# Kernel tuning notes

Hardware: AMD Instinct MI355X
Metric: run time of the kernel (lower is better)

The kernel has to match this reference:

```python
import jax, jax.numpy as jnp
import numpy as np

N = 131072        # total nodes in batched graph
E = 2097152       # total edges (avg degree 16)
F_IN = 256        # input feature dim
DIMS = [64, 32, 16]
G = 128           # number of graphs in batch


def setup_inputs() -> dict:
    key = jax.random.key(0)
    ks = jax.random.split(key, 16)
    inp = {
        "features": jax.random.normal(ks[0], (N, F_IN), jnp.float32),
        "src": jax.random.randint(ks[1], (E,), 0, N),
        "dst": jax.random.randint(ks[2], (E,), 0, N),
        "graph_ids": jnp.sort(jax.random.randint(ks[3], (N,), 0, G)),
    }
    d = F_IN
    for i, out in enumerate(DIMS):
        inp[f"W{i}"] = jax.random.normal(ks[4 + 2 * i], (d, out), jnp.float32) / np.sqrt(d).astype(np.float32)
        inp[f"b{i}"] = jax.random.normal(ks[5 + 2 * i], (out,), jnp.float32) * 0.01
        d = out
    inp["Wc"] = jax.random.normal(ks[10], (DIMS[-1], 1), jnp.float32) / np.sqrt(DIMS[-1]).astype(np.float32)
    inp["bc"] = jax.random.normal(ks[11], (1,), jnp.float32) * 0.01
    return inp


def _graph_conv(h, W, b, src, dst, src_norm, dst_norm):
    # DGL GraphConv, norm='both', activation=relu, allow_zero_in_degree=True
    # (in_feats > out_feats everywhere here, so project before aggregating)
    hw = (h * src_norm) @ W                       # [N, out]
    agg = jax.ops.segment_sum(hw[src], dst, num_segments=N)  # gather->scatter-add
    return jax.nn.relu(agg * dst_norm + b)


def reference(features, src, dst, graph_ids, W0, b0, W1, b1, W2, b2, Wc, bc):
    ones_e = jnp.ones((E,), jnp.float32)
    out_deg = jax.ops.segment_sum(ones_e, src, num_segments=N)
    in_deg = jax.ops.segment_sum(ones_e, dst, num_segments=N)
    # DGL clamps degrees to >=1 before pow(-0.5)
    src_norm = jnp.power(jnp.maximum(out_deg, 1.0), -0.5)[:, None]  # [N,1]
    dst_norm = jnp.power(jnp.maximum(in_deg, 1.0), -0.5)[:, None]

    h = features
    for W, b in ((W0, b0), (W1, b1), (W2, b2)):
        h = _graph_conv(h, W, b, src, dst, src_norm, dst_norm)

    # dgl.mean_nodes over batched graph
    sums = jax.ops.segment_sum(h, graph_ids, num_segments=G)          # [G,16]
    cnt = jax.ops.segment_sum(jnp.ones((N,), jnp.float32), graph_ids, num_segments=G)
    hg = sums / jnp.maximum(cnt, 1.0)[:, None]

    return (hg @ Wc + bc).squeeze(-1)  # [G] logits
```

## Files before the change

kernel.cpp:

```cpp
#include <hip/hip_runtime.h>

#define N_NODES 131072
#define N_EDGES 2097152
#define N_GRAPHS 128
#define POOL_NPB 256
#define NB 256
#define BUCKET_SHIFT 9
#define BUCKET_CAP 9728
#define BIN_EPT 32

__global__ __launch_bounds__(256) void k_init_buckets(int* __restrict__ cursor_d,
                                                      int* __restrict__ cursor_s) {
  int i = threadIdx.x;
  cursor_d[i] = i * BUCKET_CAP;
  cursor_s[i] = i * BUCKET_CAP;
}

__global__ __launch_bounds__(256) void k_bin(const int* __restrict__ src,
                                             const int* __restrict__ dst,
                                             int* __restrict__ cursor_d,
                                             int* __restrict__ cursor_s,
                                             unsigned int* __restrict__ recs_d,
                                             unsigned short* __restrict__ recs_s) {
  __shared__ int hd[NB];
  __shared__ int hs[NB];
  const int t = threadIdx.x;
  const int e0 = blockIdx.x * (256 * BIN_EPT);
  hd[t] = 0; hs[t] = 0;
  __syncthreads();
#pragma unroll 4
  for (int k = 0; k < BIN_EPT; ++k) {
    int e = e0 + k * 256 + t;
    atomicAdd(&hd[dst[e] >> BUCKET_SHIFT], 1);
    atomicAdd(&hs[src[e] >> BUCKET_SHIFT], 1);
  }
  __syncthreads();
  { int c = hd[t]; hd[t] = c ? atomicAdd(&cursor_d[t], c) : 0; }
  { int c = hs[t]; hs[t] = c ? atomicAdd(&cursor_s[t], c) : 0; }
  __syncthreads();
#pragma unroll 4
  for (int k = 0; k < BIN_EPT; ++k) {
    int e = e0 + k * 256 + t;
    int s = src[e];
    int d = dst[e];
    int pd = atomicAdd(&hd[d >> BUCKET_SHIFT], 1);
    recs_d[pd] = ((unsigned int)s << BUCKET_SHIFT) | (unsigned int)(d & 511);
    int ps = atomicAdd(&hs[s >> BUCKET_SHIFT], 1);
    recs_s[ps] = (unsigned short)(s & 511);
  }
}

__global__ __launch_bounds__(512) void k_outdeg(const unsigned short* __restrict__ recs_s,
                                                const int* __restrict__ cursor_s,
                                                float* __restrict__ src_norm) {
  __shared__ int hist[512];
  const int b = blockIdx.x;
  const int t = threadIdx.x;
  hist[t] = 0;
  __syncthreads();
  const int beg = b * BUCKET_CAP;
  const int end = cursor_s[b];
  for (int i = beg + t; i < end; i += 512) atomicAdd(&hist[recs_s[i]], 1);
  __syncthreads();
  int od = hist[t]; if (od < 1) od = 1;
  src_norm[b * 512 + t] = 1.0f / sqrtf((float)od);
}

__global__ __launch_bounds__(256) void k_bucket_scan(const int* __restrict__ cursor_d,
                                                     int* __restrict__ bucket_base,
                                                     int* __restrict__ row_start) {
  __shared__ int tmp[256];
  int t = threadIdx.x;
  int c = cursor_d[t] - t * BUCKET_CAP;
  tmp[t] = c;
  __syncthreads();
  for (int off = 1; off < 256; off <<= 1) {
    int x = (t >= off) ? tmp[t - off] : 0;
    __syncthreads();
    tmp[t] += x;
    __syncthreads();
  }
  bucket_base[t] = tmp[t] - c;
  if (t == 0) row_start[N_NODES] = N_EDGES;
}

__global__ __launch_bounds__(512) void k_fill2(const unsigned int* __restrict__ recs_d,
                                               const int* __restrict__ cursor_d,
                                               const int* __restrict__ bucket_base,
                                               int* __restrict__ row_start,
                                               float* __restrict__ dst_norm,
                                               int* __restrict__ csr_src) {
  __shared__ int hist[512];
  __shared__ int lcur[512];
  const int b = blockIdx.x;
  const int t = threadIdx.x;
  hist[t] = 0;
  __syncthreads();
  const int beg = b * BUCKET_CAP;
  const int end = cursor_d[b];
  for (int i = beg + t; i < end; i += 512) atomicAdd(&hist[recs_d[i] & 511], 1);
  __syncthreads();
  int deg = hist[t];
  lcur[t] = deg;
  __syncthreads();
  for (int off = 1; off < 512; off <<= 1) {
    int x = (t >= off) ? lcur[t - off] : 0;
    __syncthreads();
    lcur[t] += x;
    __syncthreads();
  }
  int rs = bucket_base[b] + lcur[t] - deg;
  row_start[b * 512 + t] = rs;
  int dd = deg < 1 ? 1 : deg;
  dst_norm[b * 512 + t] = 1.0f / sqrtf((float)dd);
  lcur[t] = rs;
  __syncthreads();
  for (int i = beg + t; i < end; i += 512) {
    unsigned int r = recs_d[i];
    int p = atomicAdd(&lcur[r & 511], 1);
    csr_src[p] = (int)(r >> BUCKET_SHIFT);
  }
}

template <int DIN, int DOUT>
__global__ __launch_bounds__(256) void k_gemm(const float* __restrict__ h,
                                              const float* __restrict__ src_norm,
                                              const float* __restrict__ W,
                                              float* __restrict__ out) {
  constexpr int KC   = 32;
  constexpr int ROWS = 128;
  constexpr int TN   = DOUT / 16;
  __shared__ float hT[KC][ROWS];
  __shared__ float Ws[KC][DOUT];

  const int t = threadIdx.x;
  const int rowBase = blockIdx.x * ROWS;
  const int tr = t & 15;
  const int tc = t >> 4;

  float acc[8][TN];
#pragma unroll
  for (int i = 0; i < 8; ++i)
#pragma unroll
    for (int j = 0; j < TN; ++j) acc[i][j] = 0.0f;

  for (int kc = 0; kc < DIN; kc += KC) {
#pragma unroll
    for (int p = 0; p < 4; ++p) {
      int rg = (t >> 3) + 32 * p;
      int ks = (t & 7) * 4;
      float4 v = *reinterpret_cast<const float4*>(&h[(size_t)(rowBase + rg) * DIN + kc + ks]);
      float nrm = src_norm[rowBase + rg];
      hT[ks + 0][rg ^ ((((ks + 0) >> 3) & 3) << 3)] = v.x * nrm;
      hT[ks + 1][rg ^ ((((ks + 1) >> 3) & 3) << 3)] = v.y * nrm;
      hT[ks + 2][rg ^ ((((ks + 2) >> 3) & 3) << 3)] = v.z * nrm;
      hT[ks + 3][rg ^ ((((ks + 3) >> 3) & 3) << 3)] = v.w * nrm;
    }
    constexpr int WEL = KC * DOUT;
#pragma unroll
    for (int base = 0; base < WEL; base += 256 * 4) {
      int idx = base + t * 4;
      if (idx < WEL) {
        int kk = idx / DOUT;
        int c  = idx % DOUT;
        *reinterpret_cast<float4*>(&Ws[kk][c]) =
            *reinterpret_cast<const float4*>(&W[(size_t)(kc + kk) * DOUT + c]);
      }
    }
    __syncthreads();
#pragma unroll
    for (int kk = 0; kk < KC; ++kk) {
      const int swz = ((kk >> 3) & 3) << 3;
      float4 a0 = *reinterpret_cast<const float4*>(&hT[kk][(tr * 4) ^ swz]);
      float4 a1 = *reinterpret_cast<const float4*>(&hT[kk][(64 + tr * 4) ^ swz]);
      float bb[TN];
#pragma unroll
      for (int j = 0; j < TN; ++j) bb[j] = Ws[kk][tc * TN + j];
      float av[8] = {a0.x, a0.y, a0.z, a0.w, a1.x, a1.y, a1.z, a1.w};
#pragma unroll
      for (int i = 0; i < 8; ++i)
#pragma unroll
        for (int j = 0; j < TN; ++j) acc[i][j] += av[i] * bb[j];
    }
    __syncthreads();
  }
#pragma unroll
  for (int half = 0; half < 2; ++half) {
#pragma unroll
    for (int i = 0; i < 4; ++i) {
      int row = rowBase + half * 64 + tr * 4 + i;
      float* op = &out[(size_t)row * DOUT + tc * TN];
      if constexpr (TN == 4) {
        float4 v = {acc[half * 4 + i][0], acc[half * 4 + i][1],
                    acc[half * 4 + i][2], acc[half * 4 + i][3]};
        *reinterpret_cast<float4*>(op) = v;
      } else if constexpr (TN == 2) {
        float2 v = {acc[half * 4 + i][0], acc[half * 4 + i][1]};
        *reinterpret_cast<float2*>(op) = v;
      } else {
        op[0] = acc[half * 4 + i][0];
      }
    }
  }
}

template <int D>
__global__ __launch_bounds__(256) void k_agg(const float* __restrict__ hw,
                                             const int* __restrict__ row_start,
                                             const int* __restrict__ csr_src,
                                             const float* __restrict__ dst_norm,
                                             const float* __restrict__ bias,
                                             float* __restrict__ out) {
  constexpr int LPN = D / 4;
  constexpr int NPW = 64 / LPN;
  const int t = threadIdx.x;
  const int lane = t & 63;
  const int wave = t >> 6;
  const int f4  = (lane % LPN) * 4;
  const int sub = lane / LPN;
  const int node = (blockIdx.x * 4 + wave) * NPW + sub;
  const int start = row_start[node];
  const int end   = row_start[node + 1];
  float ax = 0.0f, ay = 0.0f, az = 0.0f, aw = 0.0f;
  int i = start;
  for (; i + 4 <= end; i += 4) {
    int s0 = csr_src[i + 0];
    int s1 = csr_src[i + 1];
    int s2 = csr_src[i + 2];
    int s3 = csr_src[i + 3];
    float4 v0 = *reinterpret_cast<const float4*>(&hw[(size_t)s0 * D + f4]);
    float4 v1 = *reinterpret_cast<const float4*>(&hw[(size_t)s1 * D + f4]);
    float4 v2 = *reinterpret_cast<const float4*>(&hw[(size_t)s2 * D + f4]);
    float4 v3 = *reinterpret_cast<const float4*>(&hw[(size_t)s3 * D + f4]);
    ax += v0.x + v1.x + v2.x + v3.x;
    ay += v0.y + v1.y + v2.y + v3.y;
    az += v0.z + v1.z + v2.z + v3.z;
    aw += v0.w + v1.w + v2.w + v3.w;
  }
  for (; i < end; ++i) {
    float4 v = *reinterpret_cast<const float4*>(&hw[(size_t)csr_src[i] * D + f4]);
    ax += v.x; ay += v.y; az += v.z; aw += v.w;
  }
  float nrm = dst_norm[node];
  float4 b4 = *reinterpret_cast<const float4*>(&bias[f4]);
  float4 r;
  r.x = fmaxf(ax * nrm + b4.x, 0.0f);
  r.y = fmaxf(ay * nrm + b4.y, 0.0f);
  r.z = fmaxf(az * nrm + b4.z, 0.0f);
  r.w = fmaxf(aw * nrm + b4.w, 0.0f);
  *reinterpret_cast<float4*>(&out[(size_t)node * D + f4]) = r;
}

__global__ __launch_bounds__(256) void k_pool(const float* __restrict__ h3,
                                              const int* __restrict__ gid,
                                              float* __restrict__ sums,
                                              float* __restrict__ cnt) {
  const int t = threadIdx.x;
  const int f = t & 15;
  const int grp = t >> 4;
  const int base = blockIdx.x * POOL_NPB;
  float acc = 0.0f, c = 0.0f;
  int cur = gid[base + grp];
#pragma unroll 4
  for (int k = 0; k < POOL_NPB / 16; ++k) {
    int node = base + grp + k * 16;
    int g = gid[node];
    float v = h3[(size_t)node * 16 + f];
    if (g != cur) {
      atomicAdd(&sums[cur * 16 + f], acc);
      if (f == 0) atomicAdd(&cnt[cur], c);
      acc = 0.0f; c = 0.0f; cur = g;
    }
    acc += v; c += 1.0f;
  }
  atomicAdd(&sums[cur * 16 + f], acc);
  if (f == 0) atomicAdd(&cnt[cur], c);
}

__global__ __launch_bounds__(128) void k_classify(const float* __restrict__ sums,
                                                  const float* __restrict__ cnt,
                                                  const float* __restrict__ Wc,
                                                  const float* __restrict__ bc,
                                                  float* __restrict__ out) {
  int g = threadIdx.x;
  float c = cnt[g]; if (c < 1.0f) c = 1.0f;
  float acc = 0.0f;
#pragma unroll
  for (int f = 0; f < 16; ++f) acc += (sums[g * 16 + f] / c) * Wc[f];
  out[g] = acc + bc[0];
}

extern "C" void kernel_launch(void* const* d_in, const int* in_sizes, int n_in,
                              void* d_out, int out_size, void* d_ws, size_t ws_size,
                              hipStream_t stream) {
  const float* features = (const float*)d_in[0];
  const int*   src      = (const int*)d_in[1];
  const int*   dst      = (const int*)d_in[2];
  const int*   gid      = (const int*)d_in[3];
  const float* W0 = (const float*)d_in[4];
  const float* b0 = (const float*)d_in[5];
  const float* W1 = (const float*)d_in[6];
  const float* b1 = (const float*)d_in[7];
  const float* W2 = (const float*)d_in[8];
  const float* b2 = (const float*)d_in[9];
  const float* Wc = (const float*)d_in[10];
  const float* bc = (const float*)d_in[11];
  float* out = (float*)d_out;

  char* w = (char*)d_ws;
  auto alloc = [&](size_t bytes) {
    void* p = (void*)w;
    w += (bytes + 255) & ~(size_t)255;
    return p;
  };
  float* src_norm    = (float*)alloc((size_t)N_NODES * 4);
  float* dst_norm    = (float*)alloc((size_t)N_NODES * 4);
  int*   row_start   = (int*)alloc((size_t)(N_NODES + 1) * 4);
  int*   cursor_d    = (int*)alloc(NB * 4);
  int*   cursor_s    = (int*)alloc(NB * 4);
  int*   bucket_base = (int*)alloc(NB * 4);
  int*   csr_src     = (int*)alloc((size_t)N_EDGES * 4);
  float* buf0        = (float*)alloc((size_t)N_NODES * 64 * 4);
  float* buf1        = (float*)alloc((size_t)N_NODES * 64 * 4);
  float* sums        = (float*)alloc((size_t)N_GRAPHS * 16 * 4);
  float* cnt         = (float*)alloc((size_t)N_GRAPHS * 4);
  unsigned int*   recs_d = (unsigned int*)buf0;
  unsigned short* recs_s = (unsigned short*)buf1;

  hipMemsetAsync(sums, 0, (size_t)(N_GRAPHS * 16 + N_GRAPHS) * 4, stream);

  k_init_buckets<<<1, 256, 0, stream>>>(cursor_d, cursor_s);
  k_bin<<<N_EDGES / (256 * BIN_EPT), 256, 0, stream>>>(src, dst, cursor_d, cursor_s,
                                                       recs_d, recs_s);
  k_outdeg<<<NB, 512, 0, stream>>>(recs_s, cursor_s, src_norm);
  k_bucket_scan<<<1, 256, 0, stream>>>(cursor_d, bucket_base, row_start);
  k_fill2<<<NB, 512, 0, stream>>>(recs_d, cursor_d, bucket_base, row_start,
                                  dst_norm, csr_src);

  k_gemm<256, 64><<<N_NODES / 128, 256, 0, stream>>>(features, src_norm, W0, buf0);
  k_agg<64><<<N_NODES / 16, 256, 0, stream>>>(buf0, row_start, csr_src, dst_norm, b0, buf1);
  k_gemm<64, 32><<<N_NODES / 128, 256, 0, stream>>>(buf1, src_norm, W1, buf0);
  k_agg<32><<<N_NODES / 32, 256, 0, stream>>>(buf0, row_start, csr_src, dst_norm, b1, buf1);
  k_gemm<32, 16><<<N_NODES / 128, 256, 0, stream>>>(buf1, src_norm, W2, buf0);
  k_agg<16><<<N_NODES / 64, 256, 0, stream>>>(buf0, row_start, csr_src, dst_norm, b2, buf1);

  k_pool<<<N_NODES / POOL_NPB, 256, 0, stream>>>(buf1, gid, sums, cnt);
  k_classify<<<1, 128, 0, stream>>>(sums, cnt, Wc, bc, out);
}
```

Baseline: 341.8 us.

## Register-prefetch next K chunk in GEMM and double rows per block

The GEMM kernel now prefetches the next K chunk of activations and weights into registers while computing the current chunk, then writes them to LDS between barriers. The block tile grows from 128 to 256 rows, so each thread accumulates 16 rows, and the src_norm values are hoisted into registers. The goal is to hide global load latency and amortise weight loads, at the cost of more registers, more LDS and half as many blocks.

Result: slower. 893.2 us (+161.3%).

```diff
diff --git a/kernel.cpp b/kernel.cpp
--- a/kernel.cpp
+++ b/kernel.cpp
@@ -128,64 +128,99 @@
                                               const float* __restrict__ W,
                                               float* __restrict__ out) {
   constexpr int KC   = 32;
-  constexpr int ROWS = 128;
+  constexpr int ROWS = 256;
   constexpr int TN   = DOUT / 16;
+  constexpr int NCH  = DIN / KC;
+  constexpr int WEL  = KC * DOUT;
+  constexpr int WN   = (WEL + 1023) / 1024;
   __shared__ float hT[KC][ROWS];
   __shared__ float Ws[KC][DOUT];
 
-  const int t = threadIdx.x;
+  const int t  = threadIdx.x;
   const int rowBase = blockIdx.x * ROWS;
   const int tr = t & 15;
   const int tc = t >> 4;
-
-  float acc[8][TN];
-#pragma unroll
-  for (int i = 0; i < 8; ++i)
+  const int rg0 = t >> 3;
+  const int ks  = (t & 7) * 4;
+
+  float norm[8];
+#pragma unroll
+  for (int p = 0; p < 8; ++p) norm[p] = src_norm[rowBase + rg0 + 32 * p];
+
+  float4 hreg[8];
+  float4 wreg[WN];
+
+  auto load_regs = [&](int ch) {
+    const int kc = ch * KC;
+#pragma unroll
+    for (int p = 0; p < 8; ++p)
+      hreg[p] = *reinterpret_cast<const float4*>(
+          &h[(size_t)(rowBase + rg0 + 32 * p) * DIN + kc + ks]);
+#pragma unroll
+    for (int i = 0; i < WN; ++i) {
+      int idx = i * 1024 + t * 4;
+      if (idx < WEL)
+        wreg[i] = *reinterpret_cast<const float4*>(&W[(size_t)kc * DOUT + idx]);
+    }
+  };
+  auto write_lds = [&]() {
+#pragma unroll
+    for (int p = 0; p < 8; ++p) {
+      int rg = rg0 + 32 * p;
+      float nrm = norm[p];
+      hT[ks + 0][rg ^ ((((ks + 0) >> 3) & 3) << 3)] = hreg[p].x * nrm;
+      hT[ks + 1][rg ^ ((((ks + 1) >> 3) & 3) << 3)] = hreg[p].y * nrm;
+      hT[ks + 2][rg ^ ((((ks + 2) >> 3) & 3) << 3)] = hreg[p].z * nrm;
+      hT[ks + 3][rg ^ ((((ks + 3) >> 3) & 3) << 3)] = hreg[p].w * nrm;
+    }
+#pragma unroll
+    for (int i = 0; i < WN; ++i) {
+      int idx = i * 1024 + t * 4;
+      if (idx < WEL)
+        *reinterpret_cast<float4*>(&Ws[0][0] + idx) = wreg[i];
+    }
+  };
+
+  float acc[16][TN];
+#pragma unroll
+  for (int i = 0; i < 16; ++i)
 #pragma unroll
     for (int j = 0; j < TN; ++j) acc[i][j] = 0.0f;
 
-  for (int kc = 0; kc < DIN; kc += KC) {
-#pragma unroll
-    for (int p = 0; p < 4; ++p) {
-      int rg = (t >> 3) + 32 * p;
-      int ks = (t & 7) * 4;
-      float4 v = *reinterpret_cast<const float4*>(&h[(size_t)(rowBase + rg) * DIN + kc + ks]);
-      float nrm = src_norm[rowBase + rg];
-      hT[ks + 0][rg ^ ((((ks + 0) >> 3) & 3) << 3)] = v.x * nrm;
-      hT[ks + 1][rg ^ ((((ks + 1) >> 3) & 3) << 3)] = v.y * nrm;
-      hT[ks + 2][rg ^ ((((ks + 2) >> 3) & 3) << 3)] = v.z * nrm;
-      hT[ks + 3][rg ^ ((((ks + 3) >> 3) & 3) << 3)] = v.w * nrm;
-    }
-    constexpr int WEL = KC * DOUT;
-#pragma unroll
-    for (int base = 0; base < WEL; base += 256 * 4) {
-      int idx = base + t * 4;
-      if (idx < WEL) {
-        int kk = idx / DOUT;
-        int c  = idx % DOUT;
-        *reinterpret_cast<float4*>(&Ws[kk][c]) =
-            *reinterpret_cast<const float4*>(&W[(size_t)(kc + kk) * DOUT + c]);
-      }
-    }
-    __syncthreads();
+  load_regs(0);
+  write_lds();
+  __syncthreads();
+
+  for (int ch = 0; ch < NCH; ++ch) {
+    if (ch + 1 < NCH) load_regs(ch + 1);
 #pragma unroll
     for (int kk = 0; kk < KC; ++kk) {
       const int swz = ((kk >> 3) & 3) << 3;
-      float4 a0 = *reinterpret_cast<const float4*>(&hT[kk][(tr * 4) ^ swz]);
-      float4 a1 = *reinterpret_cast<const float4*>(&hT[kk][(64 + tr * 4) ^ swz]);
+      float4 a[4];
+#pragma unroll
+      for (int half = 0; half < 4; ++half)
+        a[half] = *reinterpret_cast<const float4*>(&hT[kk][((tr * 4) ^ swz) + 64 * half]);
       float bb[TN];
 #pragma unroll
       for (int j = 0; j < TN; ++j) bb[j] = Ws[kk][tc * TN + j];
-      float av[8] = {a0.x, a0.y, a0.z, a0.w, a1.x, a1.y, a1.z, a1.w};
-#pragma unroll
-      for (int i = 0; i < 8; ++i)
-#pragma unroll
-        for (int j = 0; j < TN; ++j) acc[i][j] += av[i] * bb[j];
-    }
-    __syncthreads();
-  }
-#pragma unroll
-  for (int half = 0; half < 2; ++half) {
+#pragma unroll
+      for (int half = 0; half < 4; ++half) {
+        float av[4] = {a[half].x, a[half].y, a[half].z, a[half].w};
+#pragma unroll
+        for (int i = 0; i < 4; ++i)
+#pragma unroll
+          for (int j = 0; j < TN; ++j) acc[half * 4 + i][j] += av[i] * bb[j];
+      }
+    }
+    if (ch + 1 < NCH) {
+      __syncthreads();
+      write_lds();
+      __syncthreads();
+    }
+  }
+
+#pragma unroll
+  for (int half = 0; half < 4; ++half) {
 #pragma unroll
     for (int i = 0; i < 4; ++i) {
       int row = rowBase + half * 64 + tr * 4 + i;
@@ -337,11 +372,11 @@
   k_fill2<<<NB, 512, 0, stream>>>(recs_d, cursor_d, bucket_base, row_start,
                                   dst_norm, csr_src);
 
-  k_gemm<256, 64><<<N_NODES / 128, 256, 0, stream>>>(features, src_norm, W0, buf0);
+  k_gemm<256, 64><<<N_NODES / 256, 256, 0, stream>>>(features, src_norm, W0, buf0);
   k_agg<64><<<N_NODES / 16, 256, 0, stream>>>(buf0, row_start, csr_src, dst_norm, b0, buf1);
-  k_gemm<64, 32><<<N_NODES / 128, 256, 0, stream>>>(buf1, src_norm, W1, buf0);
+  k_gemm<64, 32><<<N_NODES / 256, 256, 0, stream>>>(buf1, src_norm, W1, buf0);
   k_agg<32><<<N_NODES / 32, 256, 0, stream>>>(buf0, row_start, csr_src, dst_norm, b1, buf1);
-  k_gemm<32, 16><<<N_NODES / 128, 256, 0, stream>>>(buf1, src_norm, W2, buf0);
+  k_gemm<32, 16><<<N_NODES / 256, 256, 0, stream>>>(buf1, src_norm, W2, buf0);
   k_agg<16><<<N_NODES / 64, 256, 0, stream>>>(buf0, row_start, csr_src, dst_norm, b2, buf1);
 
   k_pool<<<N_NODES / POOL_NPB, 256, 0, stream>>>(buf1, gid, sums, cnt);
```
